# Kernel tuning notes

Hardware: AMD Instinct MI355X
Metric: run time of the kernel (lower is better)

The kernel has to match this reference:

```python
import jax, jax.numpy as jnp
import numpy as np

B, T, D, H, L = 64, 256, 64, 512, 10


def setup_inputs() -> dict:
    key = jax.random.key(0)
    ks = jax.random.split(key, 8)
    k_init = 1.0 / np.sqrt(H)  # PyTorch LSTMCell/Linear uniform init bound
    u = lambda k, shape: jax.random.uniform(k, shape, jnp.float32, -k_init, k_init)
    return {
        "x": jax.random.normal(ks[0], (B, T, D), jnp.float32),
        "W_ih0": u(ks[1], (4 * H, D)),        # layer 0 input weights
        "W_ih": u(ks[2], (L - 1, 4 * H, H)),  # layers 1..L-1 input weights
        "W_hh": u(ks[3], (L, 4 * H, H)),      # recurrent weights
        "b_ih": u(ks[4], (L, 4 * H)),
        "b_hh": u(ks[5], (L, 4 * H)),
        "W_out": u(ks[6], (D, H)),            # linear head weight
        "b_out": u(ks[7], (D,)),
    }


def _cell(x, h, c, W_i, W_h, b):
    # PyTorch LSTMCell: gates ordered (i, f, g, o)
    g = x @ W_i.T + h @ W_h.T + b  # [B, 4H]
    i, f, gg, o = jnp.split(g, 4, axis=-1)
    i = jax.nn.sigmoid(i)
    f = jax.nn.sigmoid(f)
    o = jax.nn.sigmoid(o)
    gg = jnp.tanh(gg)
    c_new = f * c + i * gg
    h_new = o * jnp.tanh(c_new)
    return h_new, c_new


def reference(x, W_ih0, W_ih, W_hh, b_ih, b_hh, W_out, b_out):
    b = b_ih + b_hh  # [L, 4H] — biases only ever appear summed

    def step(carry, x_t):
        h, c = carry  # each [L, B, H]
        h0, c0 = _cell(x_t, h[0], c[0], W_ih0, W_hh[0], b[0])
        hs, cs = [h0], [c0]
        for i in range(1, L):  # fixed small layer count
            hi, ci = _cell(hs[-1], h[i], c[i], W_ih[i - 1], W_hh[i], b[i])
            hs.append(hi)
            cs.append(ci)
        y = hs[-1] @ W_out.T + b_out  # [B, D] per-step linear head
        return (jnp.stack(hs), jnp.stack(cs)), y

    init = (jnp.zeros((L, B, H), jnp.float32), jnp.zeros((L, B, H), jnp.float32))
    _, ys = jax.lax.scan(step, init, jnp.swapaxes(x, 0, 1))  # ys: [T, B, D]
    return jnp.swapaxes(ys, 0, 1)  # [B, T, D]
```

## Files before the change

### kernel.cpp

```cpp
#include <hip/hip_runtime.h>
#include <hip/hip_fp16.h>
#include <stdint.h>

typedef _Float16 h8 __attribute__((ext_vector_type(8)));
typedef float f4 __attribute__((ext_vector_type(4)));

#define MFMA16(a,b,c) __builtin_amdgcn_mfma_f32_16x16x32_f16((a),(b),(c),0,0,0)

constexpr size_t XT_OFF = 0;
constexpr size_t XT_BYTES = 256ull * 4096 * 2;
constexpr size_t WSTRM_OFF = XT_OFF + XT_BYTES;
constexpr size_t WSTRM_BYTES = 144ull * 106496;
constexpr size_t PL_OFF = WSTRM_OFF + WSTRM_BYTES;
constexpr size_t PX_OFF = PL_OFF + 1024;
constexpr size_t CNT_OFF = PX_OFF + 1024;
constexpr size_t DIAG_OFF = CNT_OFF + 64;
constexpr size_t HL_OFF = DIAG_OFF + 4032;

__device__ __forceinline__ h8 gld16_p(const void* base, int voff) {
  h8 v; asm volatile("global_load_dwordx4 %0, %1, %2" : "=v"(v) : "v"(voff), "s"(base)); return v;
}
__device__ __forceinline__ h8 gld16_sc1(const void* base, int voff) {
  h8 v; asm volatile("global_load_dwordx4 %0, %1, %2 sc1" : "=v"(v) : "v"(voff), "s"(base)); return v;
}
__device__ __forceinline__ void gst16_p(const void* base, int voff, h8 v) {
  asm volatile("global_store_dwordx4 %0, %1, %2" :: "v"(voff), "v"(v), "s"(base) : "memory");
}
__device__ __forceinline__ void gst16_sc1(const void* base, int voff, h8 v) {
  asm volatile("global_store_dwordx4 %0, %1, %2 sc1" :: "v"(voff), "v"(v), "s"(base) : "memory");
}
#define WAITI(n) do { asm volatile("s_waitcnt vmcnt(" #n ")" ::: "memory"); \
                      __builtin_amdgcn_sched_barrier(0); } while (0)

__device__ __forceinline__ int ld_prog(const int* p) {
  return __hip_atomic_load(p, __ATOMIC_RELAXED, __HIP_MEMORY_SCOPE_AGENT);
}
#define INV_L1() asm volatile("buffer_inv sc0\n\ts_waitcnt vmcnt(0)" ::: "memory")

__device__ __forceinline__ float sigm(float x) { return __fdividef(1.f, 1.f + __expf(-x)); }
__device__ __forceinline__ float tanh_f(float x) { return 1.f - __fdividef(2.f, __expf(2.f*x) + 1.f); }

__global__ __launch_bounds__(256) void zero_kernel(char* ws, int rs) {
  int i = blockIdx.x * 256 + threadIdx.x;
  if (i < 163840) {
    int layer = i >> 14, w = i & 16383;
    ((int*)(ws + HL_OFF))[(size_t)layer * rs * 16384 + w] = 0;
  } else {
    int j = i - 163840;
    if (j < 168) ((int*)(ws + PL_OFF))[j] = -1;
    else if (j < 336) ((int*)(ws + PX_OFF))[j - 168] = -1;
    else if (j < 344) ((int*)(ws + CNT_OFF))[j - 336] = 0;
    else if (j == 344) ((int*)(ws + DIAG_OFF))[0] = 0;
  }
}

__global__ __launch_bounds__(256) void xprep_kernel(const float* __restrict__ X, char* ws) {
  int u = blockIdx.x * 256 + threadIdx.x;
  if (u >= 131072) return;
  int t = u >> 9, rem = u & 511, kg = rem >> 6, b = rem & 63;
  const float* src = X + ((size_t)b * 256 + t) * 64 + kg * 8;
  h8 v;
#pragma unroll
  for (int j = 0; j < 8; ++j) v[j] = (_Float16)src[j];
  *(h8*)(ws + XT_OFF + (size_t)u * 16) = v;
}

__global__ __launch_bounds__(256) void wsprep_kernel(const float* __restrict__ Wih,
                                                     const float* __restrict__ Whh, char* ws) {
  int u = blockIdx.x * 256 + threadIdx.x;
  if (u >= 144 * 6656) return;
  int cu = u / 6656, rem = u % 6656;
  int s = rem / 512, rem2 = rem % 512;
  int nt = rem2 >> 6, l = rem2 & 63;
  int ppc = l >> 2, lgc = l & 3;
  int L = 1 + cu / 16, cl = cu % 16, hbase = cl * 32;
  int kt = 4 + s, k = kt * 32 + lgc * 8;
  int row = (nt & 3) * 512 + hbase + ((nt >> 2) << 4) + ppc;
  const float* src = (k < 512) ? (Wih + (size_t)(L - 1) * 1048576 + (size_t)row * 512 + k)
                               : (Whh + (size_t)L * 1048576 + (size_t)row * 512 + (k - 512));
  h8 v;
#pragma unroll
  for (int j = 0; j < 8; ++j) v[j] = (_Float16)src[j];
  uint32_t off = (uint32_t)(ppc * 64 + lgc * 16) ^ (uint32_t)((ppc & 7) << 4);
  *(h8*)(ws + WSTRM_OFF + (size_t)cu * 106496 + (size_t)s * 8192 + (size_t)nt * 1024 + off) = v;
}

#define KTRES(r, Areg) do {                                                     \
  _Pragma("unroll") for (int nt_ = 0; nt_ < 8; ++nt_) {                         \
    h8 bv_ = *(const h8*)(lds + ((((r) * 8 + nt_) << 10) + swzo));              \
    acc[nt_] = MFMA16((Areg), bv_, acc[nt_]); } } while (0)

#define KTSTR(s, Areg) do {                                                     \
  _Pragma("unroll") for (int nt_ = 0; nt_ < 8; ++nt_)                           \
    acc[nt_] = MFMA16((Areg), Bst[s][nt_], acc[nt_]); } while (0)

#define ISSB(s) do { _Pragma("unroll") for (int nt_ = 0; nt_ < 8; ++nt_)        \
    Bst[s][nt_] = gld16_p(strm, (s) * 8192 + (nt_ << 10) + (int)swzo); } while (0)

#define ISSAS(i0) do { _Pragma("unroll") for (int i_ = 0; i_ < 4; ++i_)         \
    AS[(i0) + i_] = gld16_p(selb, ((i0) + i_) * 4096 + abb); } while (0)

#define SCR 155648

__global__ __launch_bounds__(256, 1) void lstm_fused(
    const float* __restrict__ X, const float* __restrict__ Wih0,
    const float* __restrict__ Wih, const float* __restrict__ Whh,
    const float* __restrict__ bih, const float* __restrict__ bhh,
    const float* __restrict__ Wout, const float* __restrict__ bout,
    float* __restrict__ out, char* __restrict__ ws, int rs)
{
  extern __shared__ char lds[];
  const int tid = threadIdx.x;
  const int lane = tid & 63;
  const int wv = tid >> 6;
  const int pp = lane & 15;
  const int lg = lane >> 4;
  const int abb = lg * 1024 + (16 * wv + pp) * 16;
  const uint32_t swzo = (uint32_t)(pp * 64 + lg * 16) ^ (uint32_t)((pp & 7) << 4);
  const int rsm = rs - 1;

  int* progL = (int*)(ws + PL_OFF);
  int* progX = (int*)(ws + PX_OFF);
  int* diag  = (int*)(ws + DIAG_OFF);
  const char* hl = ws + HL_OFF;
  const char* hx = hl + (size_t)10 * rs * 65536;

  int xcd;
  asm volatile("s_getreg_b32 %0, hwreg(HW_REG_XCC_ID)" : "=s"(xcd));
  xcd &= 7;
  if (tid == 0) {
    int s = atomicAdd((int*)(ws + CNT_OFF) + xcd, 1);
    *(int*)lds = s;
  }
  __syncthreads();
  const int slot = *(int*)lds;
  __syncthreads();

  if (xcd == 5) {
    if (slot >= 8) return;
    const int hd = slot, d0 = hd * 8;
    const float* wrow0 = Wout + (size_t)(d0 + wv) * 512;
    const float* wrow1 = Wout + (size_t)(d0 + 4 + wv) * 512;
    const int b = lane;
    const bool pv = lane < 16;
    const int* pw = progX + 144 + (lane & 15);
    for (int th = 0; th < 256; ++th) {
      if (wv == 0) {
        int it = 0; bool bailed = false;
        for (;;) {
          int v = ld_prog(pw);
          if (__ballot(!pv || v >= th) == ~0ull) break;
          __builtin_amdgcn_s_sleep(1);
          if (++it > 60000) { bailed = true; break; }
        }
        if (bailed && lane == 0) atomicMax(diag, 10000 + th);
      }
      __builtin_amdgcn_s_barrier();
      const char* h9 = hx + (size_t)(4 * rs + ((th + 1) & rsm)) * 65536;
      h8 H0[16], H1[16], H2[16], H3[16];
#pragma unroll
      for (int i = 0; i < 16; ++i) H0[i] = gld16_sc1(h9, i * 1024 + b * 16);
#pragma unroll
      for (int i = 0; i < 16; ++i) H1[i] = gld16_sc1(h9, (16 + i) * 1024 + b * 16);
      float a0 = bout[d0 + wv], a1 = bout[d0 + 4 + wv];
#define KH(kb, H) do { _Pragma("unroll") for (int i_ = 0; i_ < 16; ++i_) {      \
        h8 hv_ = H[i_]; float hf_[8];                                           \
        _Pragma("unroll") for (int j_ = 0; j_ < 8; ++j_) hf_[j_] = (float)hv_[j_]; \
        int kg_ = (kb) + i_;                                                    \
        f4 w0_ = *(const f4*)(wrow0 + kg_ * 8); f4 w1_ = *(const f4*)(wrow0 + kg_ * 8 + 4); \
        a0 += hf_[0]*w0_[0]+hf_[1]*w0_[1]+hf_[2]*w0_[2]+hf_[3]*w0_[3]           \
            + hf_[4]*w1_[0]+hf_[5]*w1_[1]+hf_[6]*w1_[2]+hf_[7]*w1_[3];          \
        f4 u0_ = *(const f4*)(wrow1 + kg_ * 8); f4 u1_ = *(const f4*)(wrow1 + kg_ * 8 + 4); \
        a1 += hf_[0]*u0_[0]+hf_[1]*u0_[1]+hf_[2]*u0_[2]+hf_[3]*u0_[3]           \
            + hf_[4]*u1_[0]+hf_[5]*u1_[1]+hf_[6]*u1_[2]+hf_[7]*u1_[3]; } } while (0)
      WAITI(16); KH(0, H0);
#pragma unroll
      for (int i = 0; i < 16; ++i) H2[i] = gld16_sc1(h9, (32 + i) * 1024 + b * 16);
      WAITI(16); KH(16, H1);
#pragma unroll
      for (int i = 0; i < 16; ++i) H3[i] = gld16_sc1(h9, (48 + i) * 1024 + b * 16);
      WAITI(16); KH(32, H2);
      WAITI(0);  KH(48, H3);
      out[(size_t)b * 16384 + (size_t)th * 64 + d0 + wv] = a0;
      out[(size_t)b * 16384 + (size_t)th * 64 + d0 + 4 + wv] = a1;
      __syncthreads();
      if (tid == 0)
        __hip_atomic_store(progX + 160 + hd, th, __ATOMIC_RELAXED, __HIP_MEMORY_SCOPE_AGENT);
    }
    if (hd == 0 && tid == 0) {
      int dv = ld_prog(diag);
      if (dv != 0) out[0] = 1.0e6f + (float)dv;
    }
    return;
  }
  if (xcd > 5 || slot >= 32) return;

  const int L = 2 * xcd + (slot >= 16);
  const int cl = slot & 15;
  const int hbase = cl * 32;
  const bool oddL = (L & 1) != 0;

  if (L == 0) {
    for (int ch = tid; ch < 9216; ch += 256) {
      int r = ch >> 9, rem = ch & 511;
      int nt = rem >> 6, l = rem & 63, ppc = l >> 2, lgc = l & 3;
      int k = r * 32 + lgc * 8;
      int row = (nt & 3) * 512 + hbase + ((nt >> 2) << 4) + ppc;
      const float* src = (k < 64) ? (Wih0 + (size_t)row * 64 + k)
                                  : (Whh + (size_t)row * 512 + (k - 64));
      h8 v;
#pragma unroll
      for (int j = 0; j < 8; ++j) v[j] = (_Float16)src[j];
      uint32_t off = (uint32_t)(ppc * 64 + lgc * 16) ^ (uint32_t)((ppc & 7) << 4);
      *(h8*)(lds + ((r * 8 + nt) << 10) + off) = v;
    }
  } else {
    const float* WihL = Wih + (size_t)(L - 1) * 1048576;
    const float* WhhL = Whh + (size_t)L * 1048576;
    for (int ch = tid; ch < 9728; ch += 256) {
      int r = ch >> 9, rem = ch & 511;
      int nt = rem >> 6, l = rem & 63, ppc = l >> 2, lgc = l & 3;
      int rkt = r < 4 ? r : r + 13;
      int k = rkt * 32 + lgc * 8;
      int row = (nt & 3) * 512 + hbase + ((nt >> 2) << 4) + ppc;
      const float* src = (k < 512) ? (WihL + (size_t)row * 512 + k)
                                   : (WhhL + (size_t)row * 512 + (k - 512));
      h8 v;
#pragma unroll
      for (int j = 0; j < 8; ++j) v[j] = (_Float16)src[j];
      uint32_t off = (uint32_t)(ppc * 64 + lgc * 16) ^ (uint32_t)((ppc & 7) << 4);
      *(h8*)(lds + ((r * 8 + nt) << 10) + off) = v;
    }
  }
  float biasv[8];
#pragma unroll
  for (int nt = 0; nt < 8; ++nt) {
    int row = (nt & 3) * 512 + hbase + ((nt >> 2) << 4) + pp;
    biasv[nt] = bih[L * 2048 + row] + bhh[L * 2048 + row];
  }
  __syncthreads();

  const int jl = lane & 15;
  bool okL = false, okX = false;
  int ixL = 0, ixX = 0, dL = 0, dX = 0;
  if (lane < 16) { okL = true; ixL = L * 16 + jl; dL = -1; }
  else if (lane < 32) {
    if (L > 0) {
      if (oddL) { okL = true; ixL = (L - 1) * 16 + jl; dL = 0; }
      else      { okX = true; ixX = (L - 1) * 16 + jl; dX = 0; }
    }
  } else if (lane < 48) {
    if (L == 9)    { if (jl < 8) { okX = true; ixX = 160 + jl; dX = -rsm; } }
    else if (oddL) { okX = true; ixX = (L + 1) * 16 + jl; dX = -rsm; }
    else           { okL = true; ixL = (L + 1) * 16 + jl; dL = -rsm; }
  }
  const volatile int* aL = (const volatile int*)(progL + ixL);
  const int* aX = progX + ixX;

  const char* strm = ws + WSTRM_OFF + (size_t)((L - 1) * 16 + cl) * 106496;
  const char* xt = ws + XT_OFF;

  float cv[2][4] = {{0,0,0,0},{0,0,0,0}};

  for (int t = 0; t < 256; ++t) {
    if (wv == 0) {
      int it = 0; bool bailed = false;
      for (;;) {
        INV_L1();
        int vL = *aL;
        int vX = ld_prog(aX);
        bool ok = (!okL || vL >= t + dL) && (!okX || vX >= t + dX);
        if (__ballot(ok) == ~0ull) break;
        if (++it > 60000) { bailed = true; break; }
        if (it > 4) __builtin_amdgcn_s_sleep(1);
      }
      if (bailed && lane == 0) atomicMax(diag, L * 1000 + t);
    }
    __builtin_amdgcn_s_barrier();

    f4 acc[8];
#pragma unroll
    for (int j = 0; j < 8; ++j) acc[j] = (f4){0.f, 0.f, 0.f, 0.f};

    if (L == 0) {
      const char* selb = hl + (size_t)(t & rsm) * 65536;
      h8 X0 = gld16_p(xt, t * 8192 + abb);
      h8 X1 = gld16_p(xt, t * 8192 + 4096 + abb);
      h8 AS[16];
#pragma unroll
      for (int i = 0; i < 16; ++i) AS[i] = gld16_p(selb, i * 4096 + abb);
      WAITI(17); KTRES(0, X0);
      WAITI(16); KTRES(1, X1);
      WAITI(15); KTRES(2, AS[0]);  WAITI(14); KTRES(3, AS[1]);
      WAITI(13); KTRES(4, AS[2]);  WAITI(12); KTRES(5, AS[3]);
      WAITI(11); KTRES(6, AS[4]);  WAITI(10); KTRES(7, AS[5]);
      WAITI(9);  KTRES(8, AS[6]);  WAITI(8);  KTRES(9, AS[7]);
      WAITI(7);  KTRES(10, AS[8]); WAITI(6);  KTRES(11, AS[9]);
      WAITI(5);  KTRES(12, AS[10]); WAITI(4); KTRES(13, AS[11]);
      WAITI(3);  KTRES(14, AS[12]); WAITI(2); KTRES(15, AS[13]);
      WAITI(1);  KTRES(16, AS[14]); WAITI(0); KTRES(17, AS[15]);
    } else {
      const char* botb = oddL ? (hl + (size_t)((L - 1) * rs + ((t + 1) & rsm)) * 65536)
                              : (hx + (size_t)(((L - 1) >> 1) * rs + ((t + 1) & rsm)) * 65536);
      const char* selb = hl + (size_t)(L * rs + (t & rsm)) * 65536;
      h8 AB[16], AS[16], Bst[13][8];
      if (oddL) {
#pragma unroll
        for (int i = 0; i < 16; ++i) AB[i] = gld16_p(botb, i * 4096 + abb);
      } else {
#pragma unroll
        for (int i = 0; i < 16; ++i) AB[i] = gld16_sc1(botb, i * 4096 + abb);
      }
      ISSB(0); ISSB(1);
      WAITI(31); KTRES(0, AB[0]); ISSB(2);
      WAITI(38); KTRES(1, AB[1]); ISSB(3);
      WAITI(45); KTRES(2, AB[2]); ISSB(4);
      WAITI(52); KTRES(3, AB[3]); ISSB(5);
      WAITI(40); KTSTR(0, AB[4]); ISSB(6);
      WAITI(40); KTSTR(1, AB[5]); ISSB(7);
      WAITI(40); KTSTR(2, AB[6]); ISSB(8);
      WAITI(40); KTSTR(3, AB[7]); ISSB(9);
      WAITI(40); KTSTR(4, AB[8]); ISSB(10);
      WAITI(40); KTSTR(5, AB[9]); ISSB(11);
      WAITI(40); KTSTR(6, AB[10]); ISSB(12);
      WAITI(40); KTSTR(7, AB[11]); ISSAS(0);
      WAITI(36); KTSTR(8, AB[12]); ISSAS(4);
      WAITI(28); KTSTR(9, AB[13]); ISSAS(8);
      WAITI(20); KTSTR(10, AB[14]); ISSAS(12);
      WAITI(12); KTSTR(11, AB[15]);
      WAITI(4);  KTSTR(12, AS[0]);
      KTRES(4, AS[1]);  KTRES(5, AS[2]);  KTRES(6, AS[3]);
      KTRES(7, AS[4]);  KTRES(8, AS[5]);  KTRES(9, AS[6]);
      KTRES(10, AS[7]); KTRES(11, AS[8]); KTRES(12, AS[9]);
      KTRES(13, AS[10]); KTRES(14, AS[11]);
      WAITI(3); KTRES(15, AS[12]);
      WAITI(2); KTRES(16, AS[13]);
      WAITI(1); KTRES(17, AS[14]);
      WAITI(0); KTRES(18, AS[15]);
    }

    const int brow = 16 * wv + 4 * lg;
#pragma unroll
    for (int jh = 0; jh < 2; ++jh) {
      const int hgl = jh * 16 + pp;
#pragma unroll
      for (int r = 0; r < 4; ++r) {
        float gi = sigm(acc[4*jh+0][r] + biasv[4*jh+0]);
        float gf = sigm(acc[4*jh+1][r] + biasv[4*jh+1]);
        float gg = tanh_f(acc[4*jh+2][r] + biasv[4*jh+2]);
        float go = sigm(acc[4*jh+3][r] + biasv[4*jh+3]);
        float cc = gf * cv[jh][r] + gi * gg;
        cv[jh][r] = cc;
        float hh = go * tanh_f(cc);
        *(_Float16*)(lds + SCR + ((hgl >> 3) << 10) + (brow + r) * 16 + ((hgl & 7) << 1))
            = (_Float16)hh;
      }
    }
    __syncthreads();
    {
      const int kg_l = tid >> 6, b = tid & 63;
      h8 vv = *(const h8*)(lds + SCR + tid * 16);
      const int goff = (((hbase >> 3) + kg_l) << 10) + b * 16;
      const char* HdL = hl + (size_t)(L * rs + ((t + 1) & rsm)) * 65536;
      gst16_p(HdL, goff, vv);
      if (oddL) {
        const char* HdX = hx + (size_t)((L >> 1) * rs + ((t + 1) & rsm)) * 65536;
        gst16_sc1(HdX, goff, vv);
      }
    }
    asm volatile("s_waitcnt vmcnt(0)" ::: "memory");
    __syncthreads();
    if (tid == 0) {
      *(volatile int*)(progL + L * 16 + cl) = t;
      __hip_atomic_store(progX + L * 16 + cl, t,
                         __ATOMIC_RELAXED, __HIP_MEMORY_SCOPE_AGENT);
    }
  }
}

extern "C" void kernel_launch(void* const* d_in, const int* in_sizes, int n_in,
                              void* d_out, int out_size, void* d_ws, size_t ws_size,
                              hipStream_t stream) {
  const float* X    = (const float*)d_in[0];
  const float* Wih0 = (const float*)d_in[1];
  const float* Wih  = (const float*)d_in[2];
  const float* Whh  = (const float*)d_in[3];
  const float* bihp = (const float*)d_in[4];
  const float* bhhp = (const float*)d_in[5];
  const float* Wout = (const float*)d_in[6];
  const float* bout = (const float*)d_in[7];
  float* out = (float*)d_out;
  char* ws = (char*)d_ws;
  (void)in_sizes; (void)n_in; (void)out_size;

  int rs = 16;
  size_t need = HL_OFF + 15ull * rs * 65536;
  if (ws_size < need) { rs = 8; need = HL_OFF + 15ull * rs * 65536; }
  if (ws_size < need) return;

  hipFuncSetAttribute((const void*)lstm_fused,
                      hipFuncAttributeMaxDynamicSharedMemorySize, 163840);

  zero_kernel<<<642, 256, 0, stream>>>(ws, rs);
  xprep_kernel<<<512, 256, 0, stream>>>(X, ws);
  wsprep_kernel<<<3744, 256, 0, stream>>>(Wih, Whh, ws);
  lstm_fused<<<256, 256, 163840, stream>>>(X, Wih0, Wih, Whh, bihp, bhhp,
                                           Wout, bout, out, ws, rs);
}
```

Baseline: 2.942 ms.

## Replace block-level barriers with per-wave progress flags in persistent LSTM pipeline

Measured after the change: 3.891 ms. +32.3%, slower.

```diff
diff --git a/kernel.cpp b/kernel.cpp
--- a/kernel.cpp
+++ b/kernel.cpp
@@ -12,10 +12,17 @@
 constexpr size_t WSTRM_OFF = XT_OFF + XT_BYTES;
 constexpr size_t WSTRM_BYTES = 144ull * 106496;
 constexpr size_t PL_OFF = WSTRM_OFF + WSTRM_BYTES;
-constexpr size_t PX_OFF = PL_OFF + 1024;
-constexpr size_t CNT_OFF = PX_OFF + 1024;
+constexpr size_t PX_OFF = PL_OFF + 4096;
+constexpr size_t CNT_OFF = PX_OFF + 4096;
 constexpr size_t DIAG_OFF = CNT_OFF + 64;
 constexpr size_t HL_OFF = DIAG_OFF + 4032;
+
+__device__ __forceinline__ const char* unif(const void* p) {
+  uint64_t u = (uint64_t)p;
+  uint32_t lo = __builtin_amdgcn_readfirstlane((uint32_t)u);
+  uint32_t hi = __builtin_amdgcn_readfirstlane((uint32_t)(u >> 32));
+  return (const char*)(((uint64_t)hi << 32) | lo);
+}
 
 __device__ __forceinline__ h8 gld16_p(const void* base, int voff) {
   h8 v; asm volatile("global_load_dwordx4 %0, %1, %2" : "=v"(v) : "v"(voff), "s"(base)); return v;
@@ -47,10 +54,10 @@
     ((int*)(ws + HL_OFF))[(size_t)layer * rs * 16384 + w] = 0;
   } else {
     int j = i - 163840;
-    if (j < 168) ((int*)(ws + PL_OFF))[j] = -1;
-    else if (j < 336) ((int*)(ws + PX_OFF))[j - 168] = -1;
-    else if (j < 344) ((int*)(ws + CNT_OFF))[j - 336] = 0;
-    else if (j == 344) ((int*)(ws + DIAG_OFF))[0] = 0;
+    if (j < 672) ((int*)(ws + PL_OFF))[j] = -1;
+    else if (j < 1344) ((int*)(ws + PX_OFF))[j - 672] = -1;
+    else if (j < 1352) ((int*)(ws + CNT_OFF))[j - 1344] = 0;
+    else if (j == 1352) ((int*)(ws + DIAG_OFF))[0] = 0;
   }
 }
 
@@ -133,7 +140,7 @@
     *(int*)lds = s;
   }
   __syncthreads();
-  const int slot = *(int*)lds;
+  const int slot = __builtin_amdgcn_readfirstlane(*(int*)lds);
   __syncthreads();
 
   if (xcd == 5) {
@@ -142,21 +149,21 @@
     const float* wrow0 = Wout + (size_t)(d0 + wv) * 512;
     const float* wrow1 = Wout + (size_t)(d0 + 4 + wv) * 512;
     const int b = lane;
-    const bool pv = lane < 16;
-    const int* pw = progX + 144 + (lane & 15);
+    const int* pw = progX + (9 * 16 + (lane >> 2)) * 4 + (lane & 3);
+    int* myf = progX + 640 + hd * 4 + wv;
     for (int th = 0; th < 256; ++th) {
-      if (wv == 0) {
+      {
         int it = 0; bool bailed = false;
         for (;;) {
           int v = ld_prog(pw);
-          if (__ballot(!pv || v >= th) == ~0ull) break;
+          if (__ballot(v >= th) == ~0ull) break;
           __builtin_amdgcn_s_sleep(1);
           if (++it > 60000) { bailed = true; break; }
         }
         if (bailed && lane == 0) atomicMax(diag, 10000 + th);
       }
-      __builtin_amdgcn_s_barrier();
-      const char* h9 = hx + (size_t)(4 * rs + ((th + 1) & rsm)) * 65536;
+      WAITI(0);
+      const char* h9 = unif(hx + (size_t)(4 * rs + ((th + 1) & rsm)) * 65536);
       h8 H0[16], H1[16], H2[16], H3[16];
 #pragma unroll
       for (int i = 0; i < 16; ++i) H0[i] = gld16_sc1(h9, i * 1024 + b * 16);
@@ -183,11 +190,10 @@
       WAITI(0);  KH(48, H3);
       out[(size_t)b * 16384 + (size_t)th * 64 + d0 + wv] = a0;
       out[(size_t)b * 16384 + (size_t)th * 64 + d0 + 4 + wv] = a1;
-      __syncthreads();
-      if (tid == 0)
-        __hip_atomic_store(progX + 160 + hd, th, __ATOMIC_RELAXED, __HIP_MEMORY_SCOPE_AGENT);
-    }
-    if (hd == 0 && tid == 0) {
+      if (lane == 0)
+        __hip_atomic_store(myf, th, __ATOMIC_RELAXED, __HIP_MEMORY_SCOPE_AGENT);
+    }
+    if (hd == 0 && wv == 0 && lane == 0) {
       int dv = ld_prog(diag);
       if (dv != 0) out[0] = 1.0e6f + (float)dv;
     }
@@ -240,52 +246,52 @@
   }
   __syncthreads();
 
-  const int jl = lane & 15;
-  bool okL = false, okX = false;
-  int ixL = 0, ixX = 0, dL = 0, dX = 0;
-  if (lane < 16) { okL = true; ixL = L * 16 + jl; dL = -1; }
-  else if (lane < 32) {
-    if (L > 0) {
-      if (oddL) { okL = true; ixL = (L - 1) * 16 + jl; dL = 0; }
-      else      { okX = true; ixX = (L - 1) * 16 + jl; dX = 0; }
-    }
-  } else if (lane < 48) {
-    if (L == 9)    { if (jl < 8) { okX = true; ixX = 160 + jl; dX = -rsm; } }
-    else if (oddL) { okX = true; ixX = (L + 1) * 16 + jl; dX = -rsm; }
-    else           { okL = true; ixL = (L + 1) * 16 + jl; dL = -rsm; }
-  }
-  const volatile int* aL = (const volatile int*)(progL + ixL);
-  const int* aX = progX + ixX;
-
-  const char* strm = ws + WSTRM_OFF + (size_t)((L - 1) * 16 + cl) * 106496;
+  const int fl = (lane >> 2);
+  const int fw = (lane & 3);
+  const volatile int* pS  = (const volatile int*)(progL + (L * 16 + fl) * 4 + fw);
+  const volatile int* pBL = (const volatile int*)(progL + ((L > 0 ? L - 1 : 0) * 16 + fl) * 4 + fw);
+  const int*          pBX = progX + ((L > 0 ? L - 1 : 0) * 16 + fl) * 4 + fw;
+  const volatile int* pCL = (const volatile int*)(progL + ((L < 9 ? L + 1 : 9) * 16 + fl) * 4 + fw);
+  const int*          pCX = (L == 9) ? (progX + 640 + (lane & 31))
+                                     : (progX + ((L + 1) * 16 + fl) * 4 + fw);
+  const bool cValid = (L != 9) || (lane < 32);
+  int* myL = progL + (L * 16 + cl) * 4 + wv;
+  int* myX = progX + (L * 16 + cl) * 4 + wv;
+
+  const char* strm = unif(ws + WSTRM_OFF + (size_t)((L - 1) * 16 + cl) * 106496);
   const char* xt = ws + XT_OFF;
 
   float cv[2][4] = {{0,0,0,0},{0,0,0,0}};
 
   for (int t = 0; t < 256; ++t) {
-    if (wv == 0) {
+    {
       int it = 0; bool bailed = false;
       for (;;) {
         INV_L1();
-        int vL = *aL;
-        int vX = ld_prog(aX);
-        bool ok = (!okL || vL >= t + dL) && (!okX || vX >= t + dX);
+        int vS = *pS;
+        int vB = (L == 0) ? 0x7fffffff : (oddL ? *pBL : ld_prog(pBX));
+        int vC;
+        if (L == 9)      vC = ld_prog(pCX);
+        else if (oddL)   vC = ld_prog(pCX);
+        else             vC = *pCL;
+        bool ok = (vS >= t - 1) && (vB >= t) && (!cValid || vC >= t - rsm);
         if (__ballot(ok) == ~0ull) break;
         if (++it > 60000) { bailed = true; break; }
         if (it > 4) __builtin_amdgcn_s_sleep(1);
       }
       if (bailed && lane == 0) atomicMax(diag, L * 1000 + t);
     }
-    __builtin_amdgcn_s_barrier();
+    WAITI(0);
 
     f4 acc[8];
 #pragma unroll
     for (int j = 0; j < 8; ++j) acc[j] = (f4){0.f, 0.f, 0.f, 0.f};
 
     if (L == 0) {
-      const char* selb = hl + (size_t)(t & rsm) * 65536;
-      h8 X0 = gld16_p(xt, t * 8192 + abb);
-      h8 X1 = gld16_p(xt, t * 8192 + 4096 + abb);
+      const char* selb = unif(hl + (size_t)(t & rsm) * 65536);
+      const char* xtb = unif(xt + (size_t)t * 8192);
+      h8 X0 = gld16_p(xtb, abb);
+      h8 X1 = gld16_p(xtb, 4096 + abb);
       h8 AS[16];
 #pragma unroll
       for (int i = 0; i < 16; ++i) AS[i] = gld16_p(selb, i * 4096 + abb);
@@ -300,9 +306,10 @@
       WAITI(3);  KTRES(14, AS[12]); WAITI(2); KTRES(15, AS[13]);
       WAITI(1);  KTRES(16, AS[14]); WAITI(0); KTRES(17, AS[15]);
     } else {
-      const char* botb = oddL ? (hl + (size_t)((L - 1) * rs + ((t + 1) & rsm)) * 65536)
-                              : (hx + (size_t)(((L - 1) >> 1) * rs + ((t + 1) & rsm)) * 65536);
-      const char* selb = hl + (size_t)(L * rs + (t & rsm)) * 65536;
+      const char* botb = unif(oddL
+          ? (hl + (size_t)((L - 1) * rs + ((t + 1) & rsm)) * 65536)
+          : (hx + (size_t)(((L - 1) >> 1) * rs + ((t + 1) & rsm)) * 65536));
+      const char* selb = unif(hl + (size_t)(L * rs + (t & rsm)) * 65536);
       h8 AB[16], AS[16], Bst[13][8];
       if (oddL) {
 #pragma unroll
@@ -339,7 +346,7 @@
       WAITI(0); KTRES(18, AS[15]);
     }
 
-    const int brow = 16 * wv + 4 * lg;
+    const int scrw = SCR + (wv << 10);
 #pragma unroll
     for (int jh = 0; jh < 2; ++jh) {
       const int hgl = jh * 16 + pp;
@@ -352,28 +359,35 @@
         float cc = gf * cv[jh][r] + gi * gg;
         cv[jh][r] = cc;
         float hh = go * tanh_f(cc);
-        *(_Float16*)(lds + SCR + ((hgl >> 3) << 10) + (brow + r) * 16 + ((hgl & 7) << 1))
+        *(_Float16*)(lds + scrw + ((hgl >> 3) << 8) + ((4 * lg + r) << 4) + ((hgl & 7) << 1))
             = (_Float16)hh;
       }
     }
-    __syncthreads();
     {
-      const int kg_l = tid >> 6, b = tid & 63;
-      h8 vv = *(const h8*)(lds + SCR + tid * 16);
-      const int goff = (((hbase >> 3) + kg_l) << 10) + b * 16;
-      const char* HdL = hl + (size_t)(L * rs + ((t + 1) & rsm)) * 65536;
+      h8 vv = *(const h8*)(lds + scrw + ((lane >> 4) << 8) + ((lane & 15) << 4));
+      const int goff = (((hbase >> 3) + (lane >> 4)) << 10) + (16 * wv + (lane & 15)) * 16;
+      const char* HdL = unif(hl + (size_t)(L * rs + ((t + 1) & rsm)) * 65536);
       gst16_p(HdL, goff, vv);
       if (oddL) {
-        const char* HdX = hx + (size_t)((L >> 1) * rs + ((t + 1) & rsm)) * 65536;
+        const char* HdX = unif(hx + (size_t)((L >> 1) * rs + ((t + 1) & rsm)) * 65536);
         gst16_sc1(HdX, goff, vv);
       }
     }
-    asm volatile("s_waitcnt vmcnt(0)" ::: "memory");
-    __syncthreads();
-    if (tid == 0) {
-      *(volatile int*)(progL + L * 16 + cl) = t;
-      __hip_atomic_store(progX + L * 16 + cl, t,
-                         __ATOMIC_RELAXED, __HIP_MEMORY_SCOPE_AGENT);
+    if (oddL) {
+      WAITI(1);
+      if (lane == 0) {
+        *(volatile int*)myL = t;
+        __builtin_amdgcn_sched_barrier(0);
+      }
+      WAITI(0);
+      if (lane == 0)
+        __hip_atomic_store(myX, t, __ATOMIC_RELAXED, __HIP_MEMORY_SCOPE_AGENT);
+    } else {
+      WAITI(0);
+      if (lane == 0) {
+        *(volatile int*)myL = t;
+        __hip_atomic_store(myX, t, __ATOMIC_RELAXED, __HIP_MEMORY_SCOPE_AGENT);
+      }
     }
   }
 }
@@ -401,7 +415,7 @@
   hipFuncSetAttribute((const void*)lstm_fused,
                       hipFuncAttributeMaxDynamicSharedMemorySize, 163840);
 
-  zero_kernel<<<642, 256, 0, stream>>>(ws, rs);
+  zero_kernel<<<646, 256, 0, stream>>>(ws, rs);
   xprep_kernel<<<512, 256, 0, stream>>>(X, ws);
   wsprep_kernel<<<3744, 256, 0, stream>>>(Wih, Whh, ws);
   lstm_fused<<<256, 256, 163840, stream>>>(X, Wih0, Wih, Whh, bihp, bhhp,
```
